# Kernel optimization log

Measured on AMD Instinct MI355X. Metric: run time of the kernel, lower is better.

Reference implementation:

```python
import jax, jax.numpy as jnp
import numpy as np

ALPHA = 0.2  # LeakyReLU negative slope
N, IN_DIM, OUT_DIM = 8192, 128, 64


def setup_inputs() -> dict:
    key = jax.random.key(0)
    k1, k2, k3, k4 = jax.random.split(key, 4)
    x = jax.random.normal(k1, (N, IN_DIM), dtype=jnp.float32)
    adj = jax.random.randint(k2, (N, N), 0, 2, dtype=jnp.int32)
    W = jax.random.normal(k3, (IN_DIM, OUT_DIM), dtype=jnp.float32) * 0.1
    a = jax.random.normal(k4, (2 * OUT_DIM, 1), dtype=jnp.float32) * 0.1
    return {"x": x, "adj": adj, "W": W, "a": a}


def reference(x, adj, W, a):
    # h = x @ W : [N, out]
    h = x @ W
    # e_ij = LeakyReLU(a^T [h_i || h_j]) computed as broadcast sum of the
    # two halves of the attention vector (avoids materializing [N,N,2*out]).
    a_src = a[:OUT_DIM, 0]   # [out]
    a_dst = a[OUT_DIM:, 0]   # [out]
    e = (h @ a_src)[:, None] + (h @ a_dst)[None, :]      # [N, N]
    e = jnp.where(e > 0, e, ALPHA * e)                    # LeakyReLU
    # mask non-edges, row-softmax
    e = jnp.where(adj > 0, e, jnp.float32(-9e15))
    attn = jax.nn.softmax(e, axis=-1)                     # [N, N]
    out = attn @ h                                        # [N, out]
    # concat=True -> ELU nonlinearity
    return jax.nn.elu(out)
```

## Files before the change

### kernel.cpp

```cpp
#include <hip/hip_runtime.h>
#include <hip/hip_bf16.h>
#include <cstdint>
#include <cstddef>

#define N_NODES 8192
#define IN_DIM  128
#define OUT_DIM 64
#define LRELU_ALPHA 0.2f
#define S_SLICES 4
#define LOG2E 1.44269504f

using f32x16 = __attribute__((ext_vector_type(16))) float;
using bf16x8 = __attribute__((ext_vector_type(8))) short;
typedef unsigned long long u64;

static __device__ __forceinline__ unsigned short f2bf(float x) {
    union { float f; unsigned u; } v; v.f = x;
    unsigned r = v.u + 0x7FFFu + ((v.u >> 16) & 1u);
    return (unsigned short)(r >> 16);
}

__global__ __launch_bounds__(256) void gat_prep(
    const float* __restrict__ x, const float* __restrict__ W,
    const float* __restrict__ a,
    float* __restrict__ svec, float* __restrict__ dvec,
    unsigned short* __restrict__ hpack)
{
    __shared__ float shA[4][8][64];
    const int tid = threadIdx.x;
    const int w   = tid >> 6;
    const int f   = tid & 63;
    const int i0  = blockIdx.x * 8;

    float acc[8];
#pragma unroll
    for (int r = 0; r < 8; ++r) acc[r] = 0.f;

    const int k0 = w * 32;
#pragma unroll 2
    for (int k = k0; k < k0 + 32; k += 4) {
        const float w0 = W[(k + 0) * OUT_DIM + f];
        const float w1 = W[(k + 1) * OUT_DIM + f];
        const float w2 = W[(k + 2) * OUT_DIM + f];
        const float w3 = W[(k + 3) * OUT_DIM + f];
#pragma unroll
        for (int r = 0; r < 8; ++r) {
            const float4 xv = *reinterpret_cast<const float4*>(
                x + (size_t)(i0 + r) * IN_DIM + k);
            acc[r] = fmaf(xv.x, w0, acc[r]);
            acc[r] = fmaf(xv.y, w1, acc[r]);
            acc[r] = fmaf(xv.z, w2, acc[r]);
            acc[r] = fmaf(xv.w, w3, acc[r]);
        }
    }
#pragma unroll
    for (int r = 0; r < 8; ++r) shA[w][r][f] = acc[r];
    __syncthreads();

    if (w == 0) {
        union { unsigned short us[8]; int4 v; } pk;
#pragma unroll
        for (int r = 0; r < 8; ++r) {
            const float hv = shA[0][r][f] + shA[1][r][f] + shA[2][r][f] + shA[3][r][f];
            pk.us[r] = f2bf(hv);
        }
        const int jb    = i0 >> 4;
        const int jhalf = (i0 >> 3) & 1;
        const int fb    = f >> 5;
        const int lidx  = (f & 31) + 32 * jhalf;
        *reinterpret_cast<int4*>(hpack + ((size_t)(jb * 2 + fb) * 64 + lidx) * 8) = pk.v;
    } else if (w == 1) {
        const float asrc = a[f];
#pragma unroll
        for (int r = 0; r < 8; ++r) {
            const float hv = shA[0][r][f] + shA[1][r][f] + shA[2][r][f] + shA[3][r][f];
            float sv = hv * asrc;
#pragma unroll
            for (int off = 32; off >= 1; off >>= 1) sv += __shfl_xor(sv, off);
            if (f == 0) svec[i0 + r] = sv * LOG2E;
        }
    } else if (w == 2) {
        const float adst = a[OUT_DIM + f];
#pragma unroll
        for (int r = 0; r < 8; ++r) {
            const float hv = shA[0][r][f] + shA[1][r][f] + shA[2][r][f] + shA[3][r][f];
            float dv = hv * adst;
#pragma unroll
            for (int off = 32; off >= 1; off >>= 1) dv += __shfl_xor(dv, off);
            if (f == 0) dvec[i0 + r] = dv * LOG2E;
        }
    }
}

__global__ __launch_bounds__(256, 2) void gat_main(
    const int* __restrict__ adj,
    const float* __restrict__ svec, const float* __restrict__ dvec,
    const unsigned short* __restrict__ hpack,
    float* __restrict__ pO, float* __restrict__ pDen)
{
    __shared__ struct { float red[4][32][64]; float redden[4][32]; } shr;

    const int tid = threadIdx.x;
    const int w   = tid >> 6;
    const int l   = tid & 63;
    const int rb  = blockIdx.x;
    const int sl  = blockIdx.y;
    const int row = l & 31;
    const int kh  = l >> 5;
    const int i0  = rb * 32;
    const int jwv = sl * 2048 + w * 512;
    const int rot = rb & 7;

    const float s_i = svec[i0 + row];
    const bf16x8* hp = reinterpret_cast<const bf16x8*>(hpack);

    struct Plains { bf16x8 b[2][4]; float4 d[2][4]; };

    auto j0of = [&](int c) { return jwv + (((c + rot) & 7) << 6); };

    auto loadAdj = [&](int (&av)[32], int c) {
        const int j0c = j0of(c);
#pragma unroll
        for (int m = 0; m < 32; ++m)
            av[m] = adj[(size_t)(i0 + m) * N_NODES + j0c + l];
    };

    auto loadPlains = [&](int c, Plains& P) {
        const int j0c = j0of(c);
#pragma unroll
        for (int ti = 0; ti < 2; ++ti) {
            const int jg = j0c + ti * 32;
            const int jb = jg >> 4;
#pragma unroll
            for (int q = 0; q < 4; ++q) P.b[ti][q] = hp[(jb * 2 + q) * 64 + l];
            const int j0 = jg + kh * 8;
            P.d[ti][0] = *reinterpret_cast<const float4*>(dvec + j0);
            P.d[ti][1] = *reinterpret_cast<const float4*>(dvec + j0 + 4);
            P.d[ti][2] = *reinterpret_cast<const float4*>(dvec + j0 + 16);
            P.d[ti][3] = *reinterpret_cast<const float4*>(dvec + j0 + 20);
        }
    };

    auto pack = [&](const int (&av)[32], unsigned& kLo, unsigned& kHi) {
        kLo = 0u; kHi = 0u;
#pragma unroll
        for (int m = 0; m < 32; ++m) {
            const u64 b = __ballot(av[m] != 0);
            if (l == m) { kLo = (unsigned)b; kHi = (unsigned)(b >> 32); }
        }
    };

    f32x16 acc0, acc1;
#pragma unroll
    for (int r = 0; r < 16; ++r) { acc0[r] = 0.f; acc1[r] = 0.f; }
    float den = 0.f;

    auto consume = [&](unsigned kLo, unsigned kHi, const Plains& P) {
        const unsigned lo32 = (unsigned)__shfl((int)kLo, row);
        const unsigned hi32 = (unsigned)__shfl((int)kHi, row);
#pragma unroll
        for (int ti = 0; ti < 2; ++ti) {
            const unsigned b32 = ti ? hi32 : lo32;
            const unsigned mq0 = b32 >> (kh * 8);
            const unsigned mq1 = b32 >> (16 + kh * 8);
            const float dd0[8] = {P.d[ti][0].x, P.d[ti][0].y, P.d[ti][0].z, P.d[ti][0].w,
                                  P.d[ti][1].x, P.d[ti][1].y, P.d[ti][1].z, P.d[ti][1].w};
            const float dd1[8] = {P.d[ti][2].x, P.d[ti][2].y, P.d[ti][2].z, P.d[ti][2].w,
                                  P.d[ti][3].x, P.d[ti][3].y, P.d[ti][3].z, P.d[ti][3].w};
            bf16x8 af0, af1;
#pragma unroll
            for (int e = 0; e < 8; ++e) {
                float ev = s_i + dd0[e];
                ev = fmaxf(ev, LRELU_ALPHA * ev);
                float pv = __builtin_amdgcn_exp2f(ev);
                pv = ((mq0 >> e) & 1u) ? pv : 0.f;
                union { float f; unsigned u; } pu; pu.f = pv;
                pu.u &= 0xFFFF0000u;
                den += pu.f;
                af0[e] = (short)(pu.u >> 16);
            }
#pragma unroll
            for (int e = 0; e < 8; ++e) {
                float ev = s_i + dd1[e];
                ev = fmaxf(ev, LRELU_ALPHA * ev);
                float pv = __builtin_amdgcn_exp2f(ev);
                pv = ((mq1 >> e) & 1u) ? pv : 0.f;
                union { float f; unsigned u; } pu; pu.f = pv;
                pu.u &= 0xFFFF0000u;
                den += pu.f;
                af1[e] = (short)(pu.u >> 16);
            }
            acc0 = __builtin_amdgcn_mfma_f32_32x32x16_bf16(af0, P.b[ti][0], acc0, 0, 0, 0);
            acc1 = __builtin_amdgcn_mfma_f32_32x32x16_bf16(af0, P.b[ti][1], acc1, 0, 0, 0);
            acc0 = __builtin_amdgcn_mfma_f32_32x32x16_bf16(af1, P.b[ti][2], acc0, 0, 0, 0);
            acc1 = __builtin_amdgcn_mfma_f32_32x32x16_bf16(af1, P.b[ti][3], acc1, 0, 0, 0);
        }
    };

    int avA[32], avB[32];
    Plains P, Q;
    unsigned kLo, kHi;

    loadAdj(avA, 0);
    asm volatile("" ::: "memory");

#pragma unroll 1
    for (int c = 0; c < 8; c += 2) {
        loadPlains(c, P);
        asm volatile("" ::: "memory");
        loadAdj(avB, c + 1);
        asm volatile("" ::: "memory");
        pack(avA, kLo, kHi);
        consume(kLo, kHi, P);
        loadPlains(c + 1, Q);
        asm volatile("" ::: "memory");
        if (c + 2 < 8) {
            loadAdj(avA, c + 2);
            asm volatile("" ::: "memory");
        }
        pack(avB, kLo, kHi);
        consume(kLo, kHi, Q);
    }

    __syncthreads();
#pragma unroll
    for (int r = 0; r < 16; ++r) {
        const int orow = (r & 3) + 8 * (r >> 2) + 4 * kh;
        shr.red[w][orow][row]      = acc0[r];
        shr.red[w][orow][32 + row] = acc1[r];
    }
    const float dtot = den + __shfl_xor(den, 32);
    if (l < 32) shr.redden[w][l] = dtot;
    __syncthreads();

    float* po = pO + ((size_t)rb * S_SLICES + sl) * 2048;
    const float* rf = &shr.red[0][0][0];
    for (int e = tid; e < 2048; e += 256)
        po[e] = rf[e] + rf[2048 + e] + rf[4096 + e] + rf[6144 + e];
    if (tid < 32) {
        pDen[((size_t)rb * S_SLICES + sl) * 32 + tid] =
            shr.redden[0][tid] + shr.redden[1][tid] +
            shr.redden[2][tid] + shr.redden[3][tid];
    }
}

__global__ __launch_bounds__(256) void gat_final(
    const float* __restrict__ pO, const float* __restrict__ pDen,
    float* __restrict__ out)
{
    const int idx = blockIdx.x * 256 + threadIdx.x;
    const int i = idx >> 6;
    const int f = idx & 63;
    const int rb = i >> 5;
    const int r  = i & 31;
    const float* po = pO + (size_t)rb * S_SLICES * 2048 + r * 64 + f;
    const float v = po[0] + po[2048] + po[4096] + po[6144];
    const float* pd = pDen + (size_t)rb * S_SLICES * 32 + r;
    const float dsum = pd[0] + pd[32] + pd[64] + pd[96];
    const float o = v / dsum;
    out[idx] = (o > 0.f) ? o : expm1f(o);
}

extern "C" void kernel_launch(void* const* d_in, const int* in_sizes, int n_in,
                              void* d_out, int out_size, void* d_ws, size_t ws_size,
                              hipStream_t stream)
{
    const float* x   = (const float*)d_in[0];
    const int*   adj = (const int*)d_in[1];
    const float* W   = (const float*)d_in[2];
    const float* a   = (const float*)d_in[3];
    float* out = (float*)d_out;

    float* svec = (float*)d_ws;
    float* dvec = svec + N_NODES;
    unsigned short* hpack = (unsigned short*)(dvec + N_NODES);
    float* pO = (float*)(hpack + (size_t)N_NODES * OUT_DIM);
    float* pDen = pO + (size_t)256 * S_SLICES * 2048;

    gat_prep<<<N_NODES / 8, 256, 0, stream>>>(x, W, a, svec, dvec, hpack);
    gat_main<<<dim3(256, S_SLICES), 256, 0, stream>>>(adj, svec, dvec, hpack, pO, pDen);
    gat_final<<<(N_NODES * OUT_DIM) / 256, 256, 0, stream>>>(pO, pDen, out);
}
```

Measured before the change: 76.94 us.

## Compress adjacency into transposed bitmask in separate kernel with permuted column order

Adds a gat_compress kernel that streams the int32 adjacency with fully coalesced int4 loads and writes per-row 64-bit ballot masks in a transposed layout. The main kernel then reads one u64 mask per row per chunk instead of 32 strided int loads plus ballots and shuffles. To match the ballot bit order, the node dimension of dvec and the packed h is permuted. This frees registers and simplifies the main loop, at the cost of an extra launch and a 8 MB bitmask write and read.

```diff
diff --git a/kernel.cpp b/kernel.cpp
--- a/kernel.cpp
+++ b/kernel.cpp
@@ -20,11 +20,15 @@
     return (unsigned short)(r >> 16);
 }
 
+static __device__ __forceinline__ int PI(int j) {
+    return (((j >> 8) << 2) + (j & 3)) * 64 + ((j & 255) >> 2);
+}
+
 __global__ __launch_bounds__(256) void gat_prep(
     const float* __restrict__ x, const float* __restrict__ W,
     const float* __restrict__ a,
-    float* __restrict__ svec, float* __restrict__ dvec,
-    unsigned short* __restrict__ hpack)
+    float* __restrict__ svec, float* __restrict__ dvecp,
+    unsigned short* __restrict__ hpackp)
 {
     __shared__ float shA[4][8][64];
     const int tid = threadIdx.x;
@@ -58,17 +62,16 @@
     __syncthreads();
 
     if (w == 0) {
-        union { unsigned short us[8]; int4 v; } pk;
+        const int fb = f >> 5;
 #pragma unroll
         for (int r = 0; r < 8; ++r) {
             const float hv = shA[0][r][f] + shA[1][r][f] + shA[2][r][f] + shA[3][r][f];
-            pk.us[r] = f2bf(hv);
-        }
-        const int jb    = i0 >> 4;
-        const int jhalf = (i0 >> 3) & 1;
-        const int fb    = f >> 5;
-        const int lidx  = (f & 31) + 32 * jhalf;
-        *reinterpret_cast<int4*>(hpack + ((size_t)(jb * 2 + fb) * 64 + lidx) * 8) = pk.v;
+            const int P  = PI(i0 + r);
+            const int jb = P >> 4;
+            const int jh = (P >> 3) & 1;
+            const int ep = P & 7;
+            hpackp[((size_t)(jb * 2 + fb) * 64 + (f & 31) + 32 * jh) * 8 + ep] = f2bf(hv);
+        }
     } else if (w == 1) {
         const float asrc = a[f];
 #pragma unroll
@@ -87,15 +90,41 @@
             float dv = hv * adst;
 #pragma unroll
             for (int off = 32; off >= 1; off >>= 1) dv += __shfl_xor(dv, off);
-            if (f == 0) dvec[i0 + r] = dv * LOG2E;
-        }
+            if (f == 0) dvecp[PI(i0 + r)] = dv * LOG2E;
+        }
+    }
+}
+
+__global__ __launch_bounds__(256) void gat_compress(
+    const int* __restrict__ adj, u64* __restrict__ bits_t)
+{
+    const int wid  = (blockIdx.x * 256 + threadIdx.x) >> 6;
+    const int l    = threadIdx.x & 63;
+    const int seg0 = wid * 32;
+
+    int4 cur = *reinterpret_cast<const int4*>(adj + (size_t)seg0 * 256 + 4 * l);
+#pragma unroll 1
+    for (int t = 0; t < 32; ++t) {
+        const int seg = seg0 + t;
+        int4 nxt = cur;
+        if (t + 1 < 32)
+            nxt = *reinterpret_cast<const int4*>(adj + (size_t)(seg + 1) * 256 + 4 * l);
+        const u64 b0 = __ballot(cur.x != 0);
+        const u64 b1 = __ballot(cur.y != 0);
+        const u64 b2 = __ballot(cur.z != 0);
+        const u64 b3 = __ballot(cur.w != 0);
+        if (l < 4) {
+            const u64 b = (l == 0) ? b0 : (l == 1) ? b1 : (l == 2) ? b2 : b3;
+            bits_t[(size_t)((seg & 31) * 4 + l) * N_NODES + (seg >> 5)] = b;
+        }
+        cur = nxt;
     }
 }
 
 __global__ __launch_bounds__(256, 2) void gat_main(
-    const int* __restrict__ adj,
-    const float* __restrict__ svec, const float* __restrict__ dvec,
-    const unsigned short* __restrict__ hpack,
+    const u64* __restrict__ bits_t,
+    const float* __restrict__ svec, const float* __restrict__ dvecp,
+    const unsigned short* __restrict__ hpackp,
     float* __restrict__ pO, float* __restrict__ pDen)
 {
     __shared__ struct { float red[4][32][64]; float redden[4][32]; } shr;
@@ -109,24 +138,19 @@
     const int kh  = l >> 5;
     const int i0  = rb * 32;
     const int jwv = sl * 2048 + w * 512;
-    const int rot = rb & 7;
+    const int wd0 = jwv >> 6;
 
     const float s_i = svec[i0 + row];
-    const bf16x8* hp = reinterpret_cast<const bf16x8*>(hpack);
+    const bf16x8* hp = reinterpret_cast<const bf16x8*>(hpackp);
 
     struct Plains { bf16x8 b[2][4]; float4 d[2][4]; };
 
-    auto j0of = [&](int c) { return jwv + (((c + rot) & 7) << 6); };
-
-    auto loadAdj = [&](int (&av)[32], int c) {
-        const int j0c = j0of(c);
-#pragma unroll
-        for (int m = 0; m < 32; ++m)
-            av[m] = adj[(size_t)(i0 + m) * N_NODES + j0c + l];
+    auto loadW = [&](int c) -> u64 {
+        return bits_t[(size_t)(wd0 + c) * N_NODES + i0 + row];
     };
 
     auto loadPlains = [&](int c, Plains& P) {
-        const int j0c = j0of(c);
+        const int j0c = jwv + c * 64;
 #pragma unroll
         for (int ti = 0; ti < 2; ++ti) {
             const int jg = j0c + ti * 32;
@@ -134,19 +158,10 @@
 #pragma unroll
             for (int q = 0; q < 4; ++q) P.b[ti][q] = hp[(jb * 2 + q) * 64 + l];
             const int j0 = jg + kh * 8;
-            P.d[ti][0] = *reinterpret_cast<const float4*>(dvec + j0);
-            P.d[ti][1] = *reinterpret_cast<const float4*>(dvec + j0 + 4);
-            P.d[ti][2] = *reinterpret_cast<const float4*>(dvec + j0 + 16);
-            P.d[ti][3] = *reinterpret_cast<const float4*>(dvec + j0 + 20);
-        }
-    };
-
-    auto pack = [&](const int (&av)[32], unsigned& kLo, unsigned& kHi) {
-        kLo = 0u; kHi = 0u;
-#pragma unroll
-        for (int m = 0; m < 32; ++m) {
-            const u64 b = __ballot(av[m] != 0);
-            if (l == m) { kLo = (unsigned)b; kHi = (unsigned)(b >> 32); }
+            P.d[ti][0] = *reinterpret_cast<const float4*>(dvecp + j0);
+            P.d[ti][1] = *reinterpret_cast<const float4*>(dvecp + j0 + 4);
+            P.d[ti][2] = *reinterpret_cast<const float4*>(dvecp + j0 + 16);
+            P.d[ti][3] = *reinterpret_cast<const float4*>(dvecp + j0 + 20);
         }
     };
 
@@ -155,9 +170,9 @@
     for (int r = 0; r < 16; ++r) { acc0[r] = 0.f; acc1[r] = 0.f; }
     float den = 0.f;
 
-    auto consume = [&](unsigned kLo, unsigned kHi, const Plains& P) {
-        const unsigned lo32 = (unsigned)__shfl((int)kLo, row);
-        const unsigned hi32 = (unsigned)__shfl((int)kHi, row);
+    auto consume = [&](u64 wv, const Plains& P) {
+        const unsigned lo32 = (unsigned)wv;
+        const unsigned hi32 = (unsigned)(wv >> 32);
 #pragma unroll
         for (int ti = 0; ti < 2; ++ti) {
             const unsigned b32 = ti ? hi32 : lo32;
@@ -197,29 +212,20 @@
         }
     };
 
-    int avA[32], avB[32];
     Plains P, Q;
-    unsigned kLo, kHi;
-
-    loadAdj(avA, 0);
-    asm volatile("" ::: "memory");
+    u64 wvA = loadW(0);
+    loadPlains(0, P);
 
 #pragma unroll 1
-    for (int c = 0; c < 8; c += 2) {
-        loadPlains(c, P);
-        asm volatile("" ::: "memory");
-        loadAdj(avB, c + 1);
-        asm volatile("" ::: "memory");
-        pack(avA, kLo, kHi);
-        consume(kLo, kHi, P);
-        loadPlains(c + 1, Q);
-        asm volatile("" ::: "memory");
-        if (c + 2 < 8) {
-            loadAdj(avA, c + 2);
-            asm volatile("" ::: "memory");
-        }
-        pack(avB, kLo, kHi);
-        consume(kLo, kHi, Q);
+    for (int c = 0; c < 8; ++c) {
+        u64 wvB = 0;
+        if (c + 1 < 8) {
+            wvB = loadW(c + 1);
+            loadPlains(c + 1, Q);
+        }
+        consume(wvA, P);
+        wvA = wvB;
+        P = Q;
     }
 
     __syncthreads();
@@ -272,12 +278,15 @@
     float* out = (float*)d_out;
 
     float* svec = (float*)d_ws;
-    float* dvec = svec + N_NODES;
-    unsigned short* hpack = (unsigned short*)(dvec + N_NODES);
-    float* pO = (float*)(hpack + (size_t)N_NODES * OUT_DIM);
+    float* dvecp = svec + N_NODES;
+    unsigned short* hpackp = (unsigned short*)(dvecp + N_NODES);
+    u64* bits_t = (u64*)(hpackp + (size_t)N_NODES * OUT_DIM);
+    float* pO = (float*)(bits_t + (size_t)128 * N_NODES);
     float* pDen = pO + (size_t)256 * S_SLICES * 2048;
 
-    gat_prep<<<N_NODES / 8, 256, 0, stream>>>(x, W, a, svec, dvec, hpack);
-    gat_main<<<dim3(256, S_SLICES), 256, 0, stream>>>(adj, svec, dvec, hpack, pO, pDen);
+    gat_prep<<<N_NODES / 8, 256, 0, stream>>>(x, W, a, svec, dvecp, hpackp);
+    gat_compress<<<2048, 256, 0, stream>>>(adj, bits_t);
+    gat_main<<<dim3(256, S_SLICES), 256, 0, stream>>>(bits_t, svec, dvecp,
+                                                      hpackp, pO, pDen);
     gat_final<<<(N_NODES * OUT_DIM) / 256, 256, 0, stream>>>(pO, pDen, out);
 }
```

Result: slower. 109.3 us (+42.1%).
